# Performance work log

Hardware: AMD Instinct MI355X
Metric: run time of the kernel (lower is better)

Reference implementation:

```python
import jax, jax.numpy as jnp
import numpy as np

LN = 8   # local_numbers
R = 2    # upscale_factor


def pixelshuffle(x, r):
    N, C, H, W = x.shape
    x = x.reshape(N, C // (r * r), r, r, H, W).transpose(0, 1, 4, 2, 5, 3)
    return x.reshape(N, C // (r * r), H * r, W * r)


def pixelunshuffle(x, r):
    N, C, H, W = x.shape
    x = x.reshape(N, C, H // r, r, W // r, r).transpose(0, 1, 3, 5, 2, 4)
    return x.reshape(N, C * r * r, H // r, W // r)


def layernorm(x, g, b):
    mu = jnp.mean(x, -1, keepdims=True)
    v = jnp.mean((x - mu) ** 2, -1, keepdims=True)
    return (x - mu) * jax.lax.rsqrt(v + 1e-5) * g + b


def mamba_fwd(x, in_w, conv_w, conv_b, xproj_w, dt_w, dt_b, A_log, Dp, out_w):
    # x: [N, L, d_model]
    d_inner = conv_w.shape[0]
    d_conv = conv_w.shape[1]
    d_state = A_log.shape[1]
    dt_rank = dt_w.shape[1]
    xz = x @ in_w.T                       # [N, L, 2*d_inner]
    xi, z = xz[..., :d_inner], xz[..., d_inner:]
    # causal depthwise conv1d
    xt = jnp.swapaxes(xi, 1, 2)           # [N, d_inner, L]
    xc = jax.lax.conv_general_dilated(
        xt, conv_w[:, None, :], (1,), [(d_conv - 1, 0)],
        feature_group_count=d_inner, dimension_numbers=('NCH', 'OIH', 'NCH'))
    xc = jax.nn.silu(jnp.swapaxes(xc + conv_b[None, :, None], 1, 2))  # [N, L, d_inner]
    x_dbl = xc @ xproj_w.T                # [N, L, dt_rank + 2*d_state]
    dt = x_dbl[..., :dt_rank]
    Bm = x_dbl[..., dt_rank:dt_rank + d_state]
    Cm = x_dbl[..., dt_rank + d_state:]
    dt = jax.nn.softplus(dt @ dt_w.T + dt_b)      # [N, L, d_inner]
    A = -jnp.exp(A_log)                            # [d_inner, d_state]
    a = jnp.exp(dt[..., None] * A)                 # [N, L, d_inner, d_state]
    b = dt[..., None] * Bm[:, :, None, :] * xc[..., None]

    def comb(l, r):
        return (l[0] * r[0], r[0] * l[1] + r[1])

    _, h = jax.lax.associative_scan(comb, (a, b), axis=1)
    y = jnp.einsum('nlds,nls->nld', h, Cm) + Dp * xc
    y = y * jax.nn.silu(z)
    return y @ out_w.T


def _make_mamba(key, d_model, d_state, d_conv, expand):
    di = expand * d_model
    dtr = max(1, (d_model + 15) // 16)
    k = jax.random.split(key, 5)
    s = 0.05
    return {
        'in_w': s * jax.random.normal(k[0], (2 * di, d_model), jnp.float32),
        'conv_w': s * jax.random.normal(k[1], (di, d_conv), jnp.float32),
        'conv_b': jnp.zeros((di,), jnp.float32),
        'xproj_w': s * jax.random.normal(k[2], (dtr + 2 * d_state, di), jnp.float32),
        'dt_w': s * jax.random.normal(k[3], (di, dtr), jnp.float32),
        'dt_b': jnp.full((di,), -4.6, jnp.float32),  # softplus(-4.6) ~ 0.01
        'A_log': jnp.log(jnp.broadcast_to(jnp.arange(1, d_state + 1, dtype=jnp.float32), (di, d_state))),
        'D': jnp.ones((di,), jnp.float32),
        'out_w': s * jax.random.normal(k[4], (d_model, di), jnp.float32),
    }


def setup_inputs() -> dict:
    key = jax.random.key(0)
    ks = jax.random.split(key, 6)
    B, C, H, W = 2, 64, 128, 128
    dm = 16  # d_model for all three modes (C//4 == H//8 == W//8 == 16)
    inp = {'x': jax.random.normal(ks[0], (B, C, H, W), jnp.float32)}
    inp['gt1'] = 0.02 * jax.random.normal(ks[1], (1, 1, dm), jnp.float32)
    inp['gt2'] = 0.02 * jax.random.normal(ks[2], (1, 1, dm), jnp.float32)
    inp['ln1_g'] = jnp.ones((dm,), jnp.float32)
    inp['ln1_b'] = jnp.zeros((dm,), jnp.float32)
    inp['ln2_g'] = jnp.ones((dm,), jnp.float32)
    inp['ln2_b'] = jnp.zeros((dm,), jnp.float32)
    for i, pfx in enumerate(['m1_', 'm2_']):
        p = _make_mamba(ks[3 + i], dm, 16, 4, 2)
        for k_, v in p.items():
            inp[pfx + k_] = v
    return inp


def reference(x, gt1, gt2, ln1_g, ln1_b, ln2_g, ln2_b,
              m1_in_w, m1_conv_w, m1_conv_b, m1_xproj_w, m1_dt_w, m1_dt_b, m1_A_log, m1_D, m1_out_w,
              m2_in_w, m2_conv_w, m2_conv_b, m2_xproj_w, m2_dt_w, m2_dt_b, m2_A_log, m2_D, m2_out_w):
    B, C, H, W = x.shape
    ch, cw = H // LN, W // LN
    nc = LN * LN
    # unfold into local chunks: [B*nc, C, ch, cw]
    xu = x.reshape(B, C, LN, ch, LN, cw).transpose(0, 2, 4, 1, 3, 5).reshape(B * nc, C, ch, cw)
    m1 = (m1_in_w, m1_conv_w, m1_conv_b, m1_xproj_w, m1_dt_w, m1_dt_b, m1_A_log, m1_D, m1_out_w)
    m2 = (m2_in_w, m2_conv_w, m2_conv_b, m2_xproj_w, m2_dt_w, m2_dt_b, m2_A_log, m2_D, m2_out_w)
    outs = []
    for mode in range(3):
        if mode == 0:
            xm = pixelshuffle(xu, R).reshape(B, nc, C // (R * R), ch * R, cw * R)
        else:
            x5 = xu.reshape(B, nc, C, ch, cw)
            xm = x5.transpose(0, 1, 3, 2, 4) if mode == 1 else x5.transpose(0, 1, 4, 2, 3)
        d, Hc, Wc = xm.shape[2], xm.shape[3], xm.shape[4]
        L = Hc * Wc
        xf = jnp.swapaxes(xm.reshape(B * nc, d, L), 1, 2)   # [B*nc, L, d]
        g = gt1 if mode == 0 else gt2
        gt = jnp.broadcast_to(g, (B * nc, g.shape[1], g.shape[2]))
        xf = jnp.concatenate([gt, xf], axis=1)
        if mode == 0:
            y = mamba_fwd(layernorm(xf, ln1_g, ln1_b), *m1)
        else:
            y = mamba_fwd(layernorm(xf, ln2_g, ln2_b), *m2)
        y = y[:, -L:, :]
        out5 = jnp.swapaxes(y, 1, 2).reshape(B, nc, d, Hc, Wc)
        if mode == 1:
            out5 = out5.transpose(0, 1, 3, 2, 4)
        elif mode == 2:
            out5 = out5.transpose(0, 1, 3, 4, 2)
        out4 = out5.reshape(B * nc, out5.shape[2], out5.shape[3], out5.shape[4])
        if mode == 0:
            out4 = pixelunshuffle(out4, R)
        Co, Ho, Wo = out4.shape[1], out4.shape[2], out4.shape[3]
        # replicate torch's view->permute->reshape reassembly exactly
        out = out4.reshape(B, nc, Co, Ho, Wo).transpose(0, 2, 1, 3, 4).reshape(B, Co, LN * Ho, LN * Wo)
        outs.append(out)
    return (outs[0] + outs[1] + outs[2]) / 3.0
```

## Files before the change

kernel.cpp:

```cpp
#include <hip/hip_runtime.h>
#include <cmath>

namespace {

constexpr int XC = 64, XH = 128, XW = 128;
constexpr int NSEQ = 128;
constexpr int TLEN = 1025;
constexpr int LSEQ = 1024;
constexpr int NCH = 16;
constexpr int CHUNK = 65;
constexpr int TT = 96;
constexpr int NT = 11;

struct MP {
    const float *in_w, *conv_w, *conv_b, *xproj_w, *dt_w, *dt_b, *A_log, *D, *out_w;
};

__device__ __forceinline__ int xidx(int b, int c, int h, int w) {
    return ((b * XC + c) * XH + h) * XW + w;
}
__device__ __forceinline__ int oidx(int b, int cube, int c, int i, int j) {
    int h = cube * 2 + (i >> 3);
    int w = ((i & 7) << 4) | j;
    return xidx(b, c, h, w);
}
__device__ __forceinline__ float siluf(float v) { return v / (1.0f + __expf(-v)); }
__device__ __forceinline__ float softplusf(float v) {
    return v > 20.0f ? v : log1pf(__expf(v));
}

template <int MODE>
__device__ __forceinline__ float gather_val(const float* __restrict__ x,
                                            const float* __restrict__ s_gt,
                                            int t, int k, int b, int bi, int bj) {
    if (t == 0) return s_gt[k];
    int l = t - 1;
    if (MODE == 0) {
        int i2 = l >> 5, j2 = l & 31;
        int h = bi * 16 + (i2 >> 1), w = bj * 16 + (j2 >> 1);
        int coff = ((i2 & 1) << 1) | (j2 & 1);
        return x[xidx(b, k * 4 + coff, h, w)];
    } else if (MODE == 1) {
        int c = l >> 4, j = l & 15;
        return x[xidx(b, c, bi * 16 + k, bj * 16 + j)];
    } else {
        int c = l >> 4, i = l & 15;
        return x[xidx(b, c, bi * 16 + i, bj * 16 + k)];
    }
}
__device__ __forceinline__ float gather_rt(int mode, const float* __restrict__ x,
                                           const float* __restrict__ s_gt,
                                           int t, int k, int b, int bi, int bj) {
    if (mode == 0) return gather_val<0>(x, s_gt, t, k, b, bi, bj);
    if (mode == 1) return gather_val<1>(x, s_gt, t, k, b, bi, bj);
    return gather_val<2>(x, s_gt, t, k, b, bi, bj);
}

template <int MODE_C>
__global__ __launch_bounds__(256) void k_p1(
    const float* __restrict__ x,
    const float* __restrict__ gt1, const float* __restrict__ gt2,
    const float* __restrict__ ln1g, const float* __restrict__ ln1b,
    const float* __restrict__ ln2g, const float* __restrict__ ln2b,
    MP P0, MP P1, int mode_base,
    float* __restrict__ ZB0, float* __restrict__ SC0, size_t arena)
{
    const int mode = (MODE_C >= 0) ? MODE_C : (mode_base + (int)blockIdx.y);
    const MP P = (mode == 0) ? P0 : P1;
    const float* gt  = (mode == 0) ? gt1 : gt2;
    const float* lng = (mode == 0) ? ln1g : ln2g;
    const float* lnb = (mode == 0) ? ln1b : ln2b;
    float* Zb = ZB0 + (size_t)blockIdx.y * arena;
    float* sc = SC0 + (size_t)blockIdx.y * arena;

    const int n = blockIdx.x / NT, tile = blockIdx.x % NT;
    const int t0 = tile * TT;
    const int ntk = min(TT, TLEN - t0);
    const int nth = ntk + 3;
    const int b = n >> 6, cube = n & 63, bi = cube >> 3, bj = cube & 7;
    const int tid = threadIdx.x;

    __shared__ __align__(16) float s_pool[TT * 37];
    float (*s_v)[17]  = (float(*)[17])s_pool;
    float (*s_xc)[37] = (float(*)[37])s_pool;
    __shared__ __align__(16) float s_xi[TT + 3][36];
    __shared__ __align__(16) float s_wT[16][64];
    __shared__ __align__(16) float s_xpT[32][36];
    __shared__ float s_xp0[32];
    __shared__ float s_cw[128], s_cb[32], s_dw[32], s_db[32];
    __shared__ float s_g[16], s_bb[16], s_gt[16];
    __shared__ float s_dt0[TT];

    for (int i = tid; i < 64 * 16; i += 256) s_wT[i & 15][i >> 4] = P.in_w[i];
    for (int i = tid; i < 33 * 32; i += 256) {
        int r = i >> 5, cc = i & 31;
        float v = P.xproj_w[i];
        if (r == 0) s_xp0[cc] = v;
        else s_xpT[cc][r - 1] = v;
    }
    if (tid < 128) s_cw[tid] = P.conv_w[tid];
    if (tid < 32) { s_cb[tid] = P.conv_b[tid]; s_dw[tid] = P.dt_w[tid]; s_db[tid] = P.dt_b[tid]; }
    if (tid < 16) { s_g[tid] = lng[tid]; s_bb[tid] = lnb[tid]; s_gt[tid] = gt[tid]; }
    __syncthreads();

    if (tid < nth) {
        int t = t0 - 3 + tid;
        float v[16];
        if (t < 0) {
#pragma unroll
            for (int k = 0; k < 16; k++) v[k] = 0.f;
        } else {
#pragma unroll
            for (int k = 0; k < 16; k++) {
                if (MODE_C >= 0) v[k] = gather_val<(MODE_C >= 0 ? MODE_C : 0)>(x, s_gt, t, k, b, bi, bj);
                else             v[k] = gather_rt(mode, x, s_gt, t, k, b, bi, bj);
            }
            float mu = 0.f;
#pragma unroll
            for (int k = 0; k < 16; k++) mu += v[k];
            mu *= (1.f / 16.f);
            float var = 0.f;
#pragma unroll
            for (int k = 0; k < 16; k++) { float d = v[k] - mu; var += d * d; }
            float inv = rsqrtf(var * (1.f / 16.f) + 1e-5f);
#pragma unroll
            for (int k = 0; k < 16; k++) v[k] = (v[k] - mu) * inv * s_g[k] + s_bb[k];
        }
#pragma unroll
        for (int k = 0; k < 16; k++) s_v[tid][k] = v[k];
    }
    __syncthreads();

    {
        const int ntt = (nth + 3) >> 2;
        for (int tl0 = tid; tl0 < ntt * 16; tl0 += 256) {
            int tt = tl0 >> 4, og = tl0 & 15;
            int oc = og * 4;
            float acc[4][4] = {{0.f}};
#pragma unroll
            for (int k = 0; k < 16; k++) {
                float4 wv = *(const float4*)&s_wT[k][oc];
                float a0 = s_v[4 * tt + 0][k];
                float a1 = s_v[4 * tt + 1][k];
                float a2 = s_v[4 * tt + 2][k];
                float a3 = s_v[4 * tt + 3][k];
                acc[0][0] += a0 * wv.x; acc[0][1] += a0 * wv.y; acc[0][2] += a0 * wv.z; acc[0][3] += a0 * wv.w;
                acc[1][0] += a1 * wv.x; acc[1][1] += a1 * wv.y; acc[1][2] += a1 * wv.z; acc[1][3] += a1 * wv.w;
                acc[2][0] += a2 * wv.x; acc[2][1] += a2 * wv.y; acc[2][2] += a2 * wv.z; acc[2][3] += a2 * wv.w;
                acc[3][0] += a3 * wv.x; acc[3][1] += a3 * wv.y; acc[3][2] += a3 * wv.z; acc[3][3] += a3 * wv.w;
            }
#pragma unroll
            for (int i = 0; i < 4; i++) {
                int tl = 4 * tt + i;
                if (tl >= nth) break;
                if (og < 8) {
                    *(float4*)&s_xi[tl][oc] =
                        make_float4(acc[i][0], acc[i][1], acc[i][2], acc[i][3]);
                } else if (tl >= 3) {
                    *(float4*)&Zb[((size_t)n * TLEN + t0 + tl - 3) * 32 + (oc - 32)] =
                        make_float4(acc[i][0], acc[i][1], acc[i][2], acc[i][3]);
                }
            }
        }
    }
    __syncthreads();

    {
        int cc = tid & 31, jg = tid >> 5;
        float c0 = s_cw[cc * 4 + 0], c1 = s_cw[cc * 4 + 1];
        float c2 = s_cw[cc * 4 + 2], c3 = s_cw[cc * 4 + 3];
        float cb = s_cb[cc];
        float* scb = sc + ((size_t)n * TLEN + t0) * 96;
        for (int j = jg; j < ntk; j += 8) {
            float acc = 0.f;
            acc += c0 * s_xi[j + 0][cc];
            acc += c1 * s_xi[j + 1][cc];
            acc += c2 * s_xi[j + 2][cc];
            acc += c3 * s_xi[j + 3][cc];
            float v = siluf(acc + cb);
            s_xc[j][cc] = v;
            scb[j * 96 + cc] = v;
        }
    }
    __syncthreads();

    {
        int qt = tid & 7, tt = tid >> 3;
        if (4 * tt < ntk) {
            float acc[4][4] = {{0.f}};
#pragma unroll
            for (int cc = 0; cc < 32; cc++) {
                float4 wv = *(const float4*)&s_xpT[cc][4 * qt];
                float a0 = s_xc[4 * tt + 0][cc];
                float a1 = s_xc[4 * tt + 1][cc];
                float a2 = s_xc[4 * tt + 2][cc];
                float a3 = s_xc[4 * tt + 3][cc];
                acc[0][0] += a0 * wv.x; acc[0][1] += a0 * wv.y; acc[0][2] += a0 * wv.z; acc[0][3] += a0 * wv.w;
                acc[1][0] += a1 * wv.x; acc[1][1] += a1 * wv.y; acc[1][2] += a1 * wv.z; acc[1][3] += a1 * wv.w;
                acc[2][0] += a2 * wv.x; acc[2][1] += a2 * wv.y; acc[2][2] += a2 * wv.z; acc[2][3] += a2 * wv.w;
                acc[3][0] += a3 * wv.x; acc[3][1] += a3 * wv.y; acc[3][2] += a3 * wv.z; acc[3][3] += a3 * wv.w;
            }
#pragma unroll
            for (int i = 0; i < 4; i++) {
                int j = 4 * tt + i;
                if (j < ntk)
                    *(float4*)&sc[((size_t)n * TLEN + t0 + j) * 96 + 64 + 4 * qt] =
                        make_float4(acc[i][0], acc[i][1], acc[i][2], acc[i][3]);
            }
        }
        if (tid < ntk) {
            float acc = 0.f;
#pragma unroll
            for (int cc = 0; cc < 32; cc++) acc += s_xc[tid][cc] * s_xp0[cc];
            s_dt0[tid] = acc;
        }
    }
    __syncthreads();

    {
        float* scb = sc + ((size_t)n * TLEN + t0) * 96;
        for (int it = tid; it < ntk * 32; it += 256) {
            int j = it >> 5, d = it & 31;
            scb[j * 96 + 32 + d] = softplusf(s_dt0[j] * s_dw[d] + s_db[d]);
        }
    }
}

template <int MODE_C>
__global__ __launch_bounds__(128) void k_scan1(
    const float* __restrict__ SC0, MP P0, MP P1, int mode_base,
    float* __restrict__ PS0, float* __restrict__ FS0, size_t arena)
{
    const int mode = (MODE_C >= 0) ? MODE_C : (mode_base + (int)blockIdx.y);
    const float* A_log = (mode == 0) ? P0.A_log : P1.A_log;
    const float* sc = SC0 + (size_t)blockIdx.y * arena;
    float* Psum = PS0 + (size_t)blockIdx.y * arena;
    float* Fsum = FS0 + (size_t)blockIdx.y * arena;

    int n = blockIdx.x >> 4;
    int c = blockIdx.x & (NCH - 1);
    int t0 = c * CHUNK;
    int nt = min(CHUNK, TLEN - t0);
    __shared__ __align__(16) float s_sc[CHUNK * 80];
    const float* src = sc + ((size_t)n * TLEN + t0) * 96;
    for (int i = threadIdx.x; i < nt * 20; i += 128) {
        int row = i / 20, q = i - row * 20;
        ((float4*)s_sc)[row * 20 + q] = *(const float4*)&src[row * 96 + q * 4];
    }
    int tid = threadIdx.x, d = tid >> 2, sg = tid & 3;
    float4 Av = *(const float4*)&A_log[d * 16 + sg * 4];
    float A0 = -__expf(Av.x), A1 = -__expf(Av.y), A2 = -__expf(Av.z), A3 = -__expf(Av.w);
    __syncthreads();
    float h0 = 0.f, h1 = 0.f, h2 = 0.f, h3 = 0.f;
    float P0v = 1.f, P1v = 1.f, P2v = 1.f, P3v = 1.f;
    for (int t = 0; t < nt; t++) {
        const float* p = s_sc + t * 80;
        float dt = p[32 + d], xc = p[d];
        float4 Bv = *(const float4*)&p[64 + sg * 4];
        float a0 = __expf(dt * A0); h0 = a0 * h0 + dt * Bv.x * xc; P0v *= a0;
        float a1 = __expf(dt * A1); h1 = a1 * h1 + dt * Bv.y * xc; P1v *= a1;
        float a2 = __expf(dt * A2); h2 = a2 * h2 + dt * Bv.z * xc; P2v *= a2;
        float a3 = __expf(dt * A3); h3 = a3 * h3 + dt * Bv.w * xc; P3v *= a3;
    }
    size_t base = ((size_t)n * NCH + c) * 512 + d * 16 + sg * 4;
    *(float4*)&Psum[base] = make_float4(P0v, P1v, P2v, P3v);
    *(float4*)&Fsum[base] = make_float4(h0, h1, h2, h3);
}

__global__ __launch_bounds__(512) void k_comb(
    const float* __restrict__ PS0, const float* __restrict__ FS0,
    float* __restrict__ HI0, size_t arena)
{
    const float* Psum = PS0 + (size_t)blockIdx.y * arena;
    const float* Fsum = FS0 + (size_t)blockIdx.y * arena;
    float* Hin = HI0 + (size_t)blockIdx.y * arena;
    int n = blockIdx.x, tid = threadIdx.x;
    const float* pb = Psum + (size_t)n * NCH * 512;
    const float* fb = Fsum + (size_t)n * NCH * 512;
    float* hb = Hin + (size_t)n * NCH * 512;
    float H = 0.f;
#pragma unroll
    for (int c = 0; c < NCH; c++) {
        float P = pb[(size_t)c * 512 + tid];
        float F = fb[(size_t)c * 512 + tid];
        hb[(size_t)c * 512 + tid] = H;
        H = F + P * H;
    }
}

template <int MODE_C>
__global__ __launch_bounds__(128) void k_scan2(
    float* __restrict__ SC0, MP P0, MP P1, int mode_base,
    const float* __restrict__ HI0, size_t arena)
{
    const int mode = (MODE_C >= 0) ? MODE_C : (mode_base + (int)blockIdx.y);
    const float* A_log = (mode == 0) ? P0.A_log : P1.A_log;
    const float* Dp = (mode == 0) ? P0.D : P1.D;
    float* sc = SC0 + (size_t)blockIdx.y * arena;
    const float* Hin = HI0 + (size_t)blockIdx.y * arena;

    int n = blockIdx.x >> 4;
    int c = blockIdx.x & (NCH - 1);
    int t0 = c * CHUNK;
    int nt = min(CHUNK, TLEN - t0);
    __shared__ __align__(16) float s_sc[CHUNK * 96];
    const float* src = sc + ((size_t)n * TLEN + t0) * 96;
    int nv4 = nt * 24;
    for (int i = threadIdx.x; i < nv4; i += 128)
        ((float4*)s_sc)[i] = ((const float4*)src)[i];
    int tid = threadIdx.x, d = tid >> 2, sg = tid & 3;
    float4 Av = *(const float4*)&A_log[d * 16 + sg * 4];
    float A0 = -__expf(Av.x), A1 = -__expf(Av.y), A2 = -__expf(Av.z), A3 = -__expf(Av.w);
    float Dd = Dp[d];
    float4 Hv = *(const float4*)&Hin[((size_t)n * NCH + c) * 512 + d * 16 + sg * 4];
    float h0 = Hv.x, h1 = Hv.y, h2 = Hv.z, h3 = Hv.w;
    __syncthreads();
    for (int t = 0; t < nt; t++) {
        float* p = s_sc + t * 96;
        float dt = p[32 + d], xc = p[d];
        float4 Bv = *(const float4*)&p[64 + sg * 4];
        float4 Cv = *(const float4*)&p[80 + sg * 4];
        float a0 = __expf(dt * A0); h0 = a0 * h0 + dt * Bv.x * xc;
        float a1 = __expf(dt * A1); h1 = a1 * h1 + dt * Bv.y * xc;
        float a2 = __expf(dt * A2); h2 = a2 * h2 + dt * Bv.z * xc;
        float a3 = __expf(dt * A3); h3 = a3 * h3 + dt * Bv.w * xc;
        float pp = h0 * Cv.x + h1 * Cv.y + h2 * Cv.z + h3 * Cv.w;
        pp += __shfl_xor(pp, 1);
        pp += __shfl_xor(pp, 2);
        if (sg == 0) p[d] = pp + Dd * xc;
    }
    __syncthreads();
    float* yb = sc + ((size_t)n * TLEN + t0) * 96;
    for (int i = threadIdx.x; i < nt * 8; i += 128) {
        int j = i >> 3, q = i & 7;
        *(float4*)&yb[j * 96 + q * 4] = *(const float4*)&s_sc[j * 96 + q * 4];
    }
}

template <int MODE>
__global__ void k_p3(const float* __restrict__ ysc, const float* __restrict__ Zb,
                     const float* __restrict__ out_w,
                     float* __restrict__ out)
{
    __shared__ float s_w[16 * 32];
    for (int i = threadIdx.x; i < 512; i += blockDim.x) s_w[i] = out_w[i];
    __syncthreads();
    int tid = blockIdx.x * blockDim.x + threadIdx.x;
    if (tid >= NSEQ * LSEQ) return;
    int n = tid >> 10, l = tid & 1023, t = l + 1;
    const float* y = ysc + ((size_t)n * TLEN + t) * 96;
    const float* z = Zb + ((size_t)n * TLEN + t) * 32;
    float yv[32];
#pragma unroll
    for (int c = 0; c < 32; c++) yv[c] = y[c] * siluf(z[c]);
    float o[16];
#pragma unroll
    for (int j = 0; j < 16; j++) {
        float acc = 0.f;
#pragma unroll
        for (int c = 0; c < 32; c++) acc += yv[c] * s_w[j * 32 + c];
        o[j] = acc * (1.0f / 3.0f);
    }
    int b = n >> 6, cube = n & 63;
    if (MODE == 0) {
        int i2 = l >> 5, j2 = l & 31;
        int io = i2 >> 1, jo = j2 >> 1;
        int coff = ((i2 & 1) << 1) | (j2 & 1);
#pragma unroll
        for (int j = 0; j < 16; j++) out[oidx(b, cube, j * 4 + coff, io, jo)] = o[j];
    } else if (MODE == 1) {
        int c = l >> 4, jj = l & 15;
#pragma unroll
        for (int j = 0; j < 16; j++) out[oidx(b, cube, c, j, jj)] += o[j];
    } else {
        int c = l >> 4, ii = l & 15;
#pragma unroll
        for (int j = 0; j < 16; j++) out[oidx(b, cube, c, ii, j)] += o[j];
    }
}

}

extern "C" void kernel_launch(void* const* d_in, const int* in_sizes, int n_in,
                              void* d_out, int out_size, void* d_ws, size_t ws_size,
                              hipStream_t stream) {
    const float* x   = (const float*)d_in[0];
    const float* gt1 = (const float*)d_in[1];
    const float* gt2 = (const float*)d_in[2];
    const float* ln1g = (const float*)d_in[3];
    const float* ln1b = (const float*)d_in[4];
    const float* ln2g = (const float*)d_in[5];
    const float* ln2b = (const float*)d_in[6];
    MP P[2];
    for (int mi = 0; mi < 2; mi++) {
        P[mi].in_w   = (const float*)d_in[7 + mi * 9 + 0];
        P[mi].conv_w = (const float*)d_in[7 + mi * 9 + 1];
        P[mi].conv_b = (const float*)d_in[7 + mi * 9 + 2];
        P[mi].xproj_w= (const float*)d_in[7 + mi * 9 + 3];
        P[mi].dt_w   = (const float*)d_in[7 + mi * 9 + 4];
        P[mi].dt_b   = (const float*)d_in[7 + mi * 9 + 5];
        P[mi].A_log  = (const float*)d_in[7 + mi * 9 + 6];
        P[mi].D      = (const float*)d_in[7 + mi * 9 + 7];
        P[mi].out_w  = (const float*)d_in[7 + mi * 9 + 8];
    }
    float* out = (float*)d_out;

    const size_t ZBs = (size_t)NSEQ * TLEN * 32;
    const size_t SCs = (size_t)NSEQ * TLEN * 96;
    const size_t PSs = (size_t)NSEQ * NCH * 512;
    const size_t arena = ZBs + SCs + 3 * PSs;

    float* A0 = (float*)d_ws;
    auto ZB = [&](int y) { return A0 + (size_t)y * arena; };
    auto SC = [&](int y) { return A0 + (size_t)y * arena + ZBs; };
    auto PS = [&](int y) { return A0 + (size_t)y * arena + ZBs + SCs; };
    auto FS = [&](int y) { return PS(y) + PSs; };
    auto HI = [&](int y) { return FS(y) + PSs; };

    const bool fits3 = ws_size >= 3 * arena * sizeof(float);
    const bool fits2 = ws_size >= 2 * arena * sizeof(float);

    dim3 b256(256), b128(128), b512(512);
    dim3 grd3((NSEQ * LSEQ + 255) / 256);

    if (fits3) {
        k_p1<-1><<<dim3(NSEQ * NT, 3), b256, 0, stream>>>(
            x, gt1, gt2, ln1g, ln1b, ln2g, ln2b, P[0], P[1], 0, ZB(0), SC(0), arena);
        k_scan1<-1><<<dim3(NSEQ * NCH, 3), b128, 0, stream>>>(
            SC(0), P[0], P[1], 0, PS(0), FS(0), arena);
        k_comb<<<dim3(NSEQ, 3), b512, 0, stream>>>(PS(0), FS(0), HI(0), arena);
        k_scan2<-1><<<dim3(NSEQ * NCH, 3), b128, 0, stream>>>(
            SC(0), P[0], P[1], 0, HI(0), arena);
        k_p3<0><<<grd3, b256, 0, stream>>>(SC(0), ZB(0), P[0].out_w, out);
        k_p3<1><<<grd3, b256, 0, stream>>>(SC(1), ZB(1), P[1].out_w, out);
        k_p3<2><<<grd3, b256, 0, stream>>>(SC(2), ZB(2), P[1].out_w, out);
    } else if (fits2) {
        k_p1<0><<<dim3(NSEQ * NT, 1), b256, 0, stream>>>(
            x, gt1, gt2, ln1g, ln1b, ln2g, ln2b, P[0], P[1], 0, ZB(0), SC(0), arena);
        k_scan1<0><<<dim3(NSEQ * NCH, 1), b128, 0, stream>>>(
            SC(0), P[0], P[1], 0, PS(0), FS(0), arena);
        k_comb<<<dim3(NSEQ, 1), b512, 0, stream>>>(PS(0), FS(0), HI(0), arena);
        k_scan2<0><<<dim3(NSEQ * NCH, 1), b128, 0, stream>>>(
            SC(0), P[0], P[1], 0, HI(0), arena);
        k_p3<0><<<grd3, b256, 0, stream>>>(SC(0), ZB(0), P[0].out_w, out);
        k_p1<-1><<<dim3(NSEQ * NT, 2), b256, 0, stream>>>(
            x, gt1, gt2, ln1g, ln1b, ln2g, ln2b, P[0], P[1], 1, ZB(0), SC(0), arena);
        k_scan1<-1><<<dim3(NSEQ * NCH, 2), b128, 0, stream>>>(
            SC(0), P[0], P[1], 1, PS(0), FS(0), arena);
        k_comb<<<dim3(NSEQ, 2), b512, 0, stream>>>(PS(0), FS(0), HI(0), arena);
        k_scan2<-1><<<dim3(NSEQ * NCH, 2), b128, 0, stream>>>(
            SC(0), P[0], P[1], 1, HI(0), arena);
        k_p3<1><<<grd3, b256, 0, stream>>>(SC(0), ZB(0), P[1].out_w, out);
        k_p3<2><<<grd3, b256, 0, stream>>>(SC(1), ZB(1), P[1].out_w, out);
    } else {
        for (int mode = 0; mode < 3; mode++) {
            if (mode == 0)
                k_p1<0><<<dim3(NSEQ * NT, 1), b256, 0, stream>>>(
                    x, gt1, gt2, ln1g, ln1b, ln2g, ln2b, P[0], P[1], 0, ZB(0), SC(0), arena);
            else if (mode == 1)
                k_p1<1><<<dim3(NSEQ * NT, 1), b256, 0, stream>>>(
                    x, gt1, gt2, ln1g, ln1b, ln2g, ln2b, P[0], P[1], 0, ZB(0), SC(0), arena);
            else
                k_p1<2><<<dim3(NSEQ * NT, 1), b256, 0, stream>>>(
                    x, gt1, gt2, ln1g, ln1b, ln2g, ln2b, P[0], P[1], 0, ZB(0), SC(0), arena);
            if (mode == 0)
                k_scan1<0><<<dim3(NSEQ * NCH, 1), b128, 0, stream>>>(SC(0), P[0], P[1], 0, PS(0), FS(0), arena);
            else if (mode == 1)
                k_scan1<1><<<dim3(NSEQ * NCH, 1), b128, 0, stream>>>(SC(0), P[0], P[1], 0, PS(0), FS(0), arena);
            else
                k_scan1<2><<<dim3(NSEQ * NCH, 1), b128, 0, stream>>>(SC(0), P[0], P[1], 0, PS(0), FS(0), arena);
            k_comb<<<dim3(NSEQ, 1), b512, 0, stream>>>(PS(0), FS(0), HI(0), arena);
            if (mode == 0)
                k_scan2<0><<<dim3(NSEQ * NCH, 1), b128, 0, stream>>>(SC(0), P[0], P[1], 0, HI(0), arena);
            else if (mode == 1)
                k_scan2<1><<<dim3(NSEQ * NCH, 1), b128, 0, stream>>>(SC(0), P[0], P[1], 0, HI(0), arena);
            else
                k_scan2<2><<<dim3(NSEQ * NCH, 1), b128, 0, stream>>>(SC(0), P[0], P[1], 0, HI(0), arena);
            if (mode == 0)      k_p3<0><<<grd3, b256, 0, stream>>>(SC(0), ZB(0), P[0].out_w, out);
            else if (mode == 1) k_p3<1><<<grd3, b256, 0, stream>>>(SC(0), ZB(0), P[1].out_w, out);
            else                k_p3<2><<<grd3, b256, 0, stream>>>(SC(0), ZB(0), P[1].out_w, out);
        }
    }
}
```

Baseline: 322.7 us.

## Store normalized inputs instead of z and recompute z projection in output kernel

The first kernel now writes the 16-wide layernormed input per token instead of the 32-wide z half of the input projection. The final kernel recomputes z from these values and the in_w rows, trading extra FLOPs for less workspace traffic. The gather is also restructured so each thread loads one element, giving coalesced loads, with layernorm done in a separate shared-memory pass. This adds an extra barrier and 16x32 MACs per token in the output kernel.

```diff
diff --git a/kernel.cpp b/kernel.cpp
--- a/kernel.cpp
+++ b/kernel.cpp
@@ -63,14 +63,14 @@
     const float* __restrict__ ln1g, const float* __restrict__ ln1b,
     const float* __restrict__ ln2g, const float* __restrict__ ln2b,
     MP P0, MP P1, int mode_base,
-    float* __restrict__ ZB0, float* __restrict__ SC0, size_t arena)
+    float* __restrict__ VB0, float* __restrict__ SC0, size_t arena)
 {
     const int mode = (MODE_C >= 0) ? MODE_C : (mode_base + (int)blockIdx.y);
     const MP P = (mode == 0) ? P0 : P1;
     const float* gt  = (mode == 0) ? gt1 : gt2;
     const float* lng = (mode == 0) ? ln1g : ln2g;
     const float* lnb = (mode == 0) ? ln1b : ln2b;
-    float* Zb = ZB0 + (size_t)blockIdx.y * arena;
+    float* VB = VB0 + (size_t)blockIdx.y * arena;
     float* sc = SC0 + (size_t)blockIdx.y * arena;
 
     const int n = blockIdx.x / NT, tile = blockIdx.x % NT;
@@ -84,14 +84,14 @@
     float (*s_v)[17]  = (float(*)[17])s_pool;
     float (*s_xc)[37] = (float(*)[37])s_pool;
     __shared__ __align__(16) float s_xi[TT + 3][36];
-    __shared__ __align__(16) float s_wT[16][64];
+    __shared__ __align__(16) float s_wT[16][32];
     __shared__ __align__(16) float s_xpT[32][36];
     __shared__ float s_xp0[32];
     __shared__ float s_cw[128], s_cb[32], s_dw[32], s_db[32];
     __shared__ float s_g[16], s_bb[16], s_gt[16];
     __shared__ float s_dt0[TT];
 
-    for (int i = tid; i < 64 * 16; i += 256) s_wT[i & 15][i >> 4] = P.in_w[i];
+    for (int i = tid; i < 32 * 16; i += 256) s_wT[i & 15][i >> 4] = P.in_w[i];
     for (int i = tid; i < 33 * 32; i += 256) {
         int r = i >> 5, cc = i & 31;
         float v = P.xproj_w[i];
@@ -103,38 +103,42 @@
     if (tid < 16) { s_g[tid] = lng[tid]; s_bb[tid] = lnb[tid]; s_gt[tid] = gt[tid]; }
     __syncthreads();
 
-    if (tid < nth) {
-        int t = t0 - 3 + tid;
-        float v[16];
-        if (t < 0) {
-#pragma unroll
-            for (int k = 0; k < 16; k++) v[k] = 0.f;
-        } else {
-#pragma unroll
-            for (int k = 0; k < 16; k++) {
-                if (MODE_C >= 0) v[k] = gather_val<(MODE_C >= 0 ? MODE_C : 0)>(x, s_gt, t, k, b, bi, bj);
-                else             v[k] = gather_rt(mode, x, s_gt, t, k, b, bi, bj);
-            }
-            float mu = 0.f;
-#pragma unroll
-            for (int k = 0; k < 16; k++) mu += v[k];
-            mu *= (1.f / 16.f);
-            float var = 0.f;
-#pragma unroll
-            for (int k = 0; k < 16; k++) { float d = v[k] - mu; var += d * d; }
-            float inv = rsqrtf(var * (1.f / 16.f) + 1e-5f);
-#pragma unroll
-            for (int k = 0; k < 16; k++) v[k] = (v[k] - mu) * inv * s_g[k] + s_bb[k];
-        }
-#pragma unroll
-        for (int k = 0; k < 16; k++) s_v[tid][k] = v[k];
+    for (int it = tid; it < nth * 16; it += 256) {
+        int tl = it >> 4, k = it & 15;
+        int t = t0 - 3 + tl;
+        float v;
+        if (t < 0) v = 0.f;
+        else if (MODE_C >= 0) v = gather_val<(MODE_C >= 0 ? MODE_C : 0)>(x, s_gt, t, k, b, bi, bj);
+        else v = gather_rt(mode, x, s_gt, t, k, b, bi, bj);
+        s_v[tl][k] = v;
+    }
+    __syncthreads();
+
+    for (int tl = tid; tl < nth; tl += 256) {
+        int t = t0 - 3 + tl;
+        if (t < 0) continue;
+        float v[16], mu = 0.f;
+#pragma unroll
+        for (int k = 0; k < 16; k++) { v[k] = s_v[tl][k]; mu += v[k]; }
+        mu *= (1.f / 16.f);
+        float var = 0.f;
+#pragma unroll
+        for (int k = 0; k < 16; k++) { float d = v[k] - mu; var += d * d; }
+        float inv = rsqrtf(var * (1.f / 16.f) + 1e-5f);
+#pragma unroll
+        for (int k = 0; k < 16; k++) s_v[tl][k] = (v[k] - mu) * inv * s_g[k] + s_bb[k];
     }
     __syncthreads();
 
     {
+        float* vb = VB + ((size_t)n * TLEN + t0) * 16;
+        for (int it = tid; it < ntk * 16; it += 256) {
+            int j = it >> 4, k = it & 15;
+            vb[it] = s_v[j + 3][k];
+        }
         const int ntt = (nth + 3) >> 2;
-        for (int tl0 = tid; tl0 < ntt * 16; tl0 += 256) {
-            int tt = tl0 >> 4, og = tl0 & 15;
+        for (int tl0 = tid; tl0 < ntt * 8; tl0 += 256) {
+            int tt = tl0 >> 3, og = tl0 & 7;
             int oc = og * 4;
             float acc[4][4] = {{0.f}};
 #pragma unroll
@@ -153,13 +157,8 @@
             for (int i = 0; i < 4; i++) {
                 int tl = 4 * tt + i;
                 if (tl >= nth) break;
-                if (og < 8) {
-                    *(float4*)&s_xi[tl][oc] =
-                        make_float4(acc[i][0], acc[i][1], acc[i][2], acc[i][3]);
-                } else if (tl >= 3) {
-                    *(float4*)&Zb[((size_t)n * TLEN + t0 + tl - 3) * 32 + (oc - 32)] =
-                        make_float4(acc[i][0], acc[i][1], acc[i][2], acc[i][3]);
-                }
+                *(float4*)&s_xi[tl][oc] =
+                    make_float4(acc[i][0], acc[i][1], acc[i][2], acc[i][3]);
             }
         }
     }
@@ -338,21 +337,35 @@
 }
 
 template <int MODE>
-__global__ void k_p3(const float* __restrict__ ysc, const float* __restrict__ Zb,
+__global__ void k_p3(const float* __restrict__ ysc, const float* __restrict__ VB,
+                     const float* __restrict__ in_w,
                      const float* __restrict__ out_w,
                      float* __restrict__ out)
 {
     __shared__ float s_w[16 * 32];
-    for (int i = threadIdx.x; i < 512; i += blockDim.x) s_w[i] = out_w[i];
+    __shared__ float s_wz[16][32];
+    for (int i = threadIdx.x; i < 512; i += blockDim.x) {
+        s_w[i] = out_w[i];
+        int oc = i >> 4, k = i & 15;
+        s_wz[k][oc] = in_w[(32 + oc) * 16 + k];
+    }
     __syncthreads();
     int tid = blockIdx.x * blockDim.x + threadIdx.x;
     if (tid >= NSEQ * LSEQ) return;
     int n = tid >> 10, l = tid & 1023, t = l + 1;
     const float* y = ysc + ((size_t)n * TLEN + t) * 96;
-    const float* z = Zb + ((size_t)n * TLEN + t) * 32;
+    const float* vv = VB + ((size_t)n * TLEN + t) * 16;
+    float v[16];
+#pragma unroll
+    for (int k = 0; k < 16; k++) v[k] = vv[k];
     float yv[32];
 #pragma unroll
-    for (int c = 0; c < 32; c++) yv[c] = y[c] * siluf(z[c]);
+    for (int c = 0; c < 32; c++) {
+        float z = 0.f;
+#pragma unroll
+        for (int k = 0; k < 16; k++) z += v[k] * s_wz[k][c];
+        yv[c] = y[c] * siluf(z);
+    }
     float o[16];
 #pragma unroll
     for (int j = 0; j < 16; j++) {
@@ -405,15 +418,15 @@
     }
     float* out = (float*)d_out;
 
-    const size_t ZBs = (size_t)NSEQ * TLEN * 32;
+    const size_t VBs = (size_t)NSEQ * TLEN * 16;
     const size_t SCs = (size_t)NSEQ * TLEN * 96;
     const size_t PSs = (size_t)NSEQ * NCH * 512;
-    const size_t arena = ZBs + SCs + 3 * PSs;
+    const size_t arena = VBs + SCs + 3 * PSs;
 
     float* A0 = (float*)d_ws;
-    auto ZB = [&](int y) { return A0 + (size_t)y * arena; };
-    auto SC = [&](int y) { return A0 + (size_t)y * arena + ZBs; };
-    auto PS = [&](int y) { return A0 + (size_t)y * arena + ZBs + SCs; };
+    auto VB = [&](int y) { return A0 + (size_t)y * arena; };
+    auto SC = [&](int y) { return A0 + (size_t)y * arena + VBs; };
+    auto PS = [&](int y) { return A0 + (size_t)y * arena + VBs + SCs; };
     auto FS = [&](int y) { return PS(y) + PSs; };
     auto HI = [&](int y) { return FS(y) + PSs; };
 
@@ -425,44 +438,44 @@
 
     if (fits3) {
         k_p1<-1><<<dim3(NSEQ * NT, 3), b256, 0, stream>>>(
-            x, gt1, gt2, ln1g, ln1b, ln2g, ln2b, P[0], P[1], 0, ZB(0), SC(0), arena);
+            x, gt1, gt2, ln1g, ln1b, ln2g, ln2b, P[0], P[1], 0, VB(0), SC(0), arena);
         k_scan1<-1><<<dim3(NSEQ * NCH, 3), b128, 0, stream>>>(
             SC(0), P[0], P[1], 0, PS(0), FS(0), arena);
         k_comb<<<dim3(NSEQ, 3), b512, 0, stream>>>(PS(0), FS(0), HI(0), arena);
         k_scan2<-1><<<dim3(NSEQ * NCH, 3), b128, 0, stream>>>(
             SC(0), P[0], P[1], 0, HI(0), arena);
-        k_p3<0><<<grd3, b256, 0, stream>>>(SC(0), ZB(0), P[0].out_w, out);
-        k_p3<1><<<grd3, b256, 0, stream>>>(SC(1), ZB(1), P[1].out_w, out);
-        k_p3<2><<<grd3, b256, 0, stream>>>(SC(2), ZB(2), P[1].out_w, out);
+        k_p3<0><<<grd3, b256, 0, stream>>>(SC(0), VB(0), P[0].in_w, P[0].out_w, out);
+        k_p3<1><<<grd3, b256, 0, stream>>>(SC(1), VB(1), P[1].in_w, P[1].out_w, out);
+        k_p3<2><<<grd3, b256, 0, stream>>>(SC(2), VB(2), P[1].in_w, P[1].out_w, out);
     } else if (fits2) {
         k_p1<0><<<dim3(NSEQ * NT, 1), b256, 0, stream>>>(
-            x, gt1, gt2, ln1g, ln1b, ln2g, ln2b, P[0], P[1], 0, ZB(0), SC(0), arena);
+            x, gt1, gt2, ln1g, ln1b, ln2g, ln2b, P[0], P[1], 0, VB(0), SC(0), arena);
         k_scan1<0><<<dim3(NSEQ * NCH, 1), b128, 0, stream>>>(
             SC(0), P[0], P[1], 0, PS(0), FS(0), arena);
         k_comb<<<dim3(NSEQ, 1), b512, 0, stream>>>(PS(0), FS(0), HI(0), arena);
         k_scan2<0><<<dim3(NSEQ * NCH, 1), b128, 0, stream>>>(
             SC(0), P[0], P[1], 0, HI(0), arena);
-        k_p3<0><<<grd3, b256, 0, stream>>>(SC(0), ZB(0), P[0].out_w, out);
+        k_p3<0><<<grd3, b256, 0, stream>>>(SC(0), VB(0), P[0].in_w, P[0].out_w, out);
         k_p1<-1><<<dim3(NSEQ * NT, 2), b256, 0, stream>>>(
-            x, gt1, gt2, ln1g, ln1b, ln2g, ln2b, P[0], P[1], 1, ZB(0), SC(0), arena);
+            x, gt1, gt2, ln1g, ln1b, ln2g, ln2b, P[0], P[1], 1, VB(0), SC(0), arena);
         k_scan1<-1><<<dim3(NSEQ * NCH, 2), b128, 0, stream>>>(
             SC(0), P[0], P[1], 1, PS(0), FS(0), arena);
         k_comb<<<dim3(NSEQ, 2), b512, 0, stream>>>(PS(0), FS(0), HI(0), arena);
         k_scan2<-1><<<dim3(NSEQ * NCH, 2), b128, 0, stream>>>(
             SC(0), P[0], P[1], 1, HI(0), arena);
-        k_p3<1><<<grd3, b256, 0, stream>>>(SC(0), ZB(0), P[1].out_w, out);
-        k_p3<2><<<grd3, b256, 0, stream>>>(SC(1), ZB(1), P[1].out_w, out);
+        k_p3<1><<<grd3, b256, 0, stream>>>(SC(0), VB(0), P[1].in_w, P[1].out_w, out);
+        k_p3<2><<<grd3, b256, 0, stream>>>(SC(1), VB(1), P[1].in_w, P[1].out_w, out);
     } else {
         for (int mode = 0; mode < 3; mode++) {
             if (mode == 0)
                 k_p1<0><<<dim3(NSEQ * NT, 1), b256, 0, stream>>>(
-                    x, gt1, gt2, ln1g, ln1b, ln2g, ln2b, P[0], P[1], 0, ZB(0), SC(0), arena);
+                    x, gt1, gt2, ln1g, ln1b, ln2g, ln2b, P[0], P[1], 0, VB(0), SC(0), arena);
             else if (mode == 1)
                 k_p1<1><<<dim3(NSEQ * NT, 1), b256, 0, stream>>>(
-                    x, gt1, gt2, ln1g, ln1b, ln2g, ln2b, P[0], P[1], 0, ZB(0), SC(0), arena);
+                    x, gt1, gt2, ln1g, ln1b, ln2g, ln2b, P[0], P[1], 0, VB(0), SC(0), arena);
             else
                 k_p1<2><<<dim3(NSEQ * NT, 1), b256, 0, stream>>>(
-                    x, gt1, gt2, ln1g, ln1b, ln2g, ln2b, P[0], P[1], 0, ZB(0), SC(0), arena);
+                    x, gt1, gt2, ln1g, ln1b, ln2g, ln2b, P[0], P[1], 0, VB(0), SC(0), arena);
             if (mode == 0)
                 k_scan1<0><<<dim3(NSEQ * NCH, 1), b128, 0, stream>>>(SC(0), P[0], P[1], 0, PS(0), FS(0), arena);
             else if (mode == 1)
@@ -476,9 +489,9 @@
                 k_scan2<1><<<dim3(NSEQ * NCH, 1), b128, 0, stream>>>(SC(0), P[0], P[1], 0, HI(0), arena);
             else
                 k_scan2<2><<<dim3(NSEQ * NCH, 1), b128, 0, stream>>>(SC(0), P[0], P[1], 0, HI(0), arena);
-            if (mode == 0)      k_p3<0><<<grd3, b256, 0, stream>>>(SC(0), ZB(0), P[0].out_w, out);
-            else if (mode == 1) k_p3<1><<<grd3, b256, 0, stream>>>(SC(0), ZB(0), P[1].out_w, out);
-            else                k_p3<2><<<grd3, b256, 0, stream>>>(SC(0), ZB(0), P[1].out_w, out);
-        }
-    }
-}
+            if (mode == 0)      k_p3<0><<<grd3, b256, 0, stream>>>(SC(0), VB(0), P[0].in_w, P[0].out_w, out);
+            else if (mode == 1) k_p3<1><<<grd3, b256, 0, stream>>>(SC(0), VB(0), P[1].in_w, P[1].out_w, out);
+            else                k_p3<2><<<grd3, b256, 0, stream>>>(SC(0), VB(0), P[1].in_w, P[1].out_w, out);
+        }
+    }
+}
```

New measurement: 308.8 us. 4.3% less time.
